# Kernel tuning notes

Measured on AMD Instinct MI355X. Metric: run time of the kernel, lower is better.

Reference implementation:

```python
import jax, jax.numpy as jnp
import numpy as np

N, D, C = 131072, 256, 1000
EPS = 1e-6


def setup_inputs() -> dict:
    key = jax.random.key(0)
    k1, k2, k3, k4 = jax.random.split(key, 4)
    feats = jax.random.normal(k1, (N, D), dtype=jnp.float32)
    pseudo_lbls = jax.random.randint(k2, (N,), 0, C)
    src_proto = jax.random.normal(k3, (C, D), dtype=jnp.float32)
    # uniform in [0.5, 1.5) to keep the Mahalanobis denominator well-conditioned
    src_proto_cov = jax.random.uniform(k4, (C, D), dtype=jnp.float32) + 0.5
    return {"feats": feats, "pseudo_lbls": pseudo_lbls,
            "src_proto": src_proto, "src_proto_cov": src_proto_cov}


def reference(feats, pseudo_lbls, src_proto, src_proto_cov):
    # Fused scatter-mean over classes (replaces the python loop over unique labels).
    num_classes, feat_dim = src_proto.shape
    counts = jax.ops.segment_sum(jnp.ones((feats.shape[0],), feats.dtype),
                                 pseudo_lbls, num_segments=num_classes)  # [C]
    sums = jax.ops.segment_sum(feats, pseudo_lbls, num_segments=num_classes)  # [C, D]
    means = sums / jnp.maximum(counts, 1.0)[:, None]                      # [C, D]
    present = counts > 0                                                  # [C]
    # GSSLoss: mean over the [n_uniq, D] elements of (mean - proto)^2 / (cov + eps)
    per_elem = (means - src_proto) ** 2 / (src_proto_cov + EPS)           # [C, D]
    per_elem = jnp.where(present[:, None], per_elem, 0.0)
    n_present = jnp.sum(present.astype(feats.dtype))
    loss = jnp.sum(per_elem) / (n_present * feat_dim)
    return loss
```

## Files before the change

### kernel.cpp

```cpp
#include <hip/hip_runtime.h>

#define EPS 1e-6f
#define MAX_C 1000
#define W 32
#define TR 128
#define RPC 4096
#define SBLK 1024


__device__ __forceinline__ void dma16(const float* g, float* l) {
    __builtin_amdgcn_global_load_lds(
        (const __attribute__((address_space(1))) unsigned int*)g,
        (__attribute__((address_space(3))) unsigned int*)l, 16, 0, 0);
}
__device__ __forceinline__ void dma4(const int* g, int* l) {
    __builtin_amdgcn_global_load_lds(
        (const __attribute__((address_space(1))) unsigned int*)g,
        (__attribute__((address_space(3))) unsigned int*)l, 4, 0, 0);
}

__global__ __launch_bounds__(SBLK)
void stream_kernel(const float* __restrict__ feats,
                   const int* __restrict__ lbls,
                   float* __restrict__ partials,
                   int* __restrict__ counts,
                   int n, int d, int nslices, int c_total) {
    int slice = blockIdx.x % nslices;
    int chunk = blockIdx.x / nslices;
    int t    = threadIdx.x;
    int wv   = t >> 6;
    int lane = t & 63;
    int half = lane >> 5;
    int col  = lane & 31;

    __shared__ float acc[MAX_C * W];
    __shared__ float stage[2][TR * W];
    __shared__ int   lbl_s[2][TR];

    int cW = c_total * W;
    int base = chunk * RPC;
    int rows = RPC; if (base + rows > n) rows = n - base;
    if (rows < 0) rows = 0;
    int ntiles = (rows + TR - 1) / TR;

    const float* fbase = feats + (size_t)base * d + slice * W;
    const int*   lbase = lbls + base;

    for (int i = t; i < cW; i += SBLK) acc[i] = 0.0f;

    if (slice == 0) {
        int* hist = (int*)&stage[0][0];
        for (int i = t; i < c_total; i += SBLK) hist[i] = 0;
        __syncthreads();
        for (int i = t; i < rows; i += SBLK) atomicAdd(&hist[lbase[i]], 1);
        __syncthreads();
        for (int i = t; i < c_total; i += SBLK) {
            int h = hist[i];
            if (h) atomicAdd(&counts[i], h);
        }
    }
    __syncthreads();

    int drow = wv * 8 + (lane >> 3);
    int dcol = (lane & 7) * 4;
    auto issue_dma = [&](int tile, int buf) {
        int r = tile * TR + drow; if (r > rows - 1) r = rows - 1;
        dma16(fbase + (size_t)r * d + dcol, &stage[buf][wv * 256]);
        if (wv == 0) {
            int r0 = tile * TR + lane;       if (r0 > rows - 1) r0 = rows - 1;
            int r1 = tile * TR + 64 + lane;  if (r1 > rows - 1) r1 = rows - 1;
            dma4(lbase + r0, &lbl_s[buf][0]);
            dma4(lbase + r1, &lbl_s[buf][64]);
        }
    };

    if (ntiles > 0) issue_dma(0, 0);

    for (int tile = 0; tile < ntiles; ++tile) {
        int cur = tile & 1;
        asm volatile("s_waitcnt vmcnt(0)" ::: "memory");
        __builtin_amdgcn_s_barrier();
        if (tile + 1 < ntiles) issue_dma(tile + 1, cur ^ 1);

        const float* stg = &stage[cur][0];
        int tb = tile * TR;
        int l0 = lbl_s[cur][lane];
        int l1 = lbl_s[cur][64 + lane];
        unsigned long long m0 = __ballot((tb + lane      < rows) && ((l0 & 15) == wv));
        unsigned long long m1 = __ballot((tb + 64 + lane < rows) && ((l1 & 15) == wv));

#define RUN(mask, lv, rbase)                                              \
        while (mask) {                                                    \
            int bA = (int)__ffsll(mask) - 1; mask &= mask - 1;            \
            int bB = -1;                                                  \
            if (mask) { bB = (int)__ffsll(mask) - 1; mask &= mask - 1; }  \
            int lA = __shfl(lv, bA);                                      \
            int lB = (bB >= 0) ? __shfl(lv, bB) : -1;                     \
            if (bB >= 0 && lB == lA) {                                    \
                if (half == 0) {                                          \
                    float v = stg[(rbase + bA) * W + col]                 \
                            + stg[(rbase + bB) * W + col];                \
                    acc[lA * W + col] += v;                               \
                }                                                         \
            } else {                                                      \
                int b_ = half ? bB : bA;                                  \
                int l_ = half ? lB : lA;                                  \
                if (b_ >= 0)                                              \
                    acc[l_ * W + col] += stg[(rbase + b_) * W + col];     \
            }                                                             \
        }
        RUN(m0, l0, 0)
        RUN(m1, l1, 64)
#undef RUN
    }
    __syncthreads();

    float* pbase = partials + (size_t)chunk * c_total * d + slice * W;
    for (int i = t; i < cW; i += SBLK) {
        int cls = i >> 5;
        int cc  = i & (W - 1);
        pbase[(size_t)cls * d + cc] = acc[i];
    }
}

__global__ __launch_bounds__(256)
void finalize_kernel(const float* __restrict__ partials,
                     const int* __restrict__ counts,
                     const float* __restrict__ proto,
                     const float* __restrict__ cov,
                     float* __restrict__ loss_acc,
                     float* __restrict__ npres_acc,
                     int* __restrict__ done,
                     float* __restrict__ out, int c_total, int d, int nchunks) {
    int c = blockIdx.x;
    int t = threadIdx.x;
    size_t idx = (size_t)c * d + t;
    size_t cstride = (size_t)c_total * d;

    float a = 0.0f;
    for (int k = 0; k < nchunks; ++k)
        a += partials[(size_t)k * cstride + idx];

    int cnt = counts[c];
    float present = (cnt > 0) ? 1.0f : 0.0f;
    float mean = a / fmaxf((float)cnt, 1.0f);
    float diff = mean - proto[idx];
    float pe = present * diff * diff / (cov[idx] + EPS);

    for (int off = 32; off > 0; off >>= 1)
        pe += __shfl_down(pe, off, 64);
    __shared__ float s[4];
    if ((t & 63) == 0) s[t >> 6] = pe;
    __syncthreads();
    if (t == 0) {
        atomicAdd(loss_acc, (s[0] + s[1]) + (s[2] + s[3]));
        atomicAdd(npres_acc, present);
        __threadfence();
        int prev = atomicAdd(done, 1);
        if (prev == c_total - 1) {
            float L = atomicAdd(loss_acc, 0.0f);
            float P = atomicAdd(npres_acc, 0.0f);
            out[0] = L / (P * (float)d);
        }
    }
}

extern "C" void kernel_launch(void* const* d_in, const int* in_sizes, int n_in,
                              void* d_out, int out_size, void* d_ws, size_t ws_size,
                              hipStream_t stream) {
    const float* feats = (const float*)d_in[0];
    const int*   lbls  = (const int*)d_in[1];
    const float* proto = (const float*)d_in[2];
    const float* cov   = (const float*)d_in[3];

    int n_rows = in_sizes[1];
    int d      = in_sizes[0] / n_rows;
    int c      = in_sizes[2] / d;

    int*   counts    = (int*)d_ws;
    float* loss_acc  = (float*)d_ws + c;
    float* npres_acc = loss_acc + 1;
    int*   done      = (int*)d_ws + c + 2;
    float* partials  = (float*)d_ws + c + 3;

    hipMemsetAsync(d_ws, 0, ((size_t)c + 3) * sizeof(int), stream);

    int nslices = d / W;
    int nchunks = (n_rows + RPC - 1) / RPC;
    stream_kernel<<<nslices * nchunks, SBLK, 0, stream>>>(
        feats, lbls, partials, counts, n_rows, d, nslices, c);
    finalize_kernel<<<c, 256, 0, stream>>>(partials, counts, proto, cov,
                                           loss_acc, npres_acc, done,
                                           (float*)d_out, c, d, nchunks);
}
```

Baseline: 270.5 us.

## Replace ballot-serialized class scatter with LDS atomics and a class-rotated layout

```diff
diff --git a/kernel.cpp b/kernel.cpp
--- a/kernel.cpp
+++ b/kernel.cpp
@@ -30,8 +30,8 @@
     int t    = threadIdx.x;
     int wv   = t >> 6;
     int lane = t & 63;
-    int half = lane >> 5;
-    int col  = lane & 31;
+    int lr   = lane >> 3;
+    int g    = lane & 7;
 
     __shared__ float acc[MAX_C * W];
     __shared__ float stage[2][TR * W];
@@ -61,11 +61,10 @@
     }
     __syncthreads();
 
-    int drow = wv * 8 + (lane >> 3);
-    int dcol = (lane & 7) * 4;
+    int drow = wv * 8 + lr;
     auto issue_dma = [&](int tile, int buf) {
         int r = tile * TR + drow; if (r > rows - 1) r = rows - 1;
-        dma16(fbase + (size_t)r * d + dcol, &stage[buf][wv * 256]);
+        dma16(fbase + (size_t)r * d + g * 4, &stage[buf][wv * 256]);
         if (wv == 0) {
             int r0 = tile * TR + lane;       if (r0 > rows - 1) r0 = rows - 1;
             int r1 = tile * TR + 64 + lane;  if (r1 > rows - 1) r1 = rows - 1;
@@ -82,44 +81,25 @@
         __builtin_amdgcn_s_barrier();
         if (tile + 1 < ntiles) issue_dma(tile + 1, cur ^ 1);
 
-        const float* stg = &stage[cur][0];
-        int tb = tile * TR;
-        int l0 = lbl_s[cur][lane];
-        int l1 = lbl_s[cur][64 + lane];
-        unsigned long long m0 = __ballot((tb + lane      < rows) && ((l0 & 15) == wv));
-        unsigned long long m1 = __ballot((tb + 64 + lane < rows) && ((l1 & 15) == wv));
-
-#define RUN(mask, lv, rbase)                                              \
-        while (mask) {                                                    \
-            int bA = (int)__ffsll(mask) - 1; mask &= mask - 1;            \
-            int bB = -1;                                                  \
-            if (mask) { bB = (int)__ffsll(mask) - 1; mask &= mask - 1; }  \
-            int lA = __shfl(lv, bA);                                      \
-            int lB = (bB >= 0) ? __shfl(lv, bB) : -1;                     \
-            if (bB >= 0 && lB == lA) {                                    \
-                if (half == 0) {                                          \
-                    float v = stg[(rbase + bA) * W + col]                 \
-                            + stg[(rbase + bB) * W + col];                \
-                    acc[lA * W + col] += v;                               \
-                }                                                         \
-            } else {                                                      \
-                int b_ = half ? bB : bA;                                  \
-                int l_ = half ? lB : lA;                                  \
-                if (b_ >= 0)                                              \
-                    acc[l_ * W + col] += stg[(rbase + b_) * W + col];     \
-            }                                                             \
+        int rglob = tile * TR + drow;
+        if (rglob < rows) {
+            float4 v = *(const float4*)&stage[cur][drow * W + g * 4];
+            int lab = lbl_s[cur][drow];
+            int b_ = lab * W, c_ = g * 4 + lab;
+            atomicAdd(&acc[b_ + ((c_ + 0) & (W - 1))], v.x);
+            atomicAdd(&acc[b_ + ((c_ + 1) & (W - 1))], v.y);
+            atomicAdd(&acc[b_ + ((c_ + 2) & (W - 1))], v.z);
+            atomicAdd(&acc[b_ + ((c_ + 3) & (W - 1))], v.w);
         }
-        RUN(m0, l0, 0)
-        RUN(m1, l1, 64)
-#undef RUN
     }
     __syncthreads();
 
     float* pbase = partials + (size_t)chunk * c_total * d + slice * W;
     for (int i = t; i < cW; i += SBLK) {
-        int cls = i >> 5;
-        int cc  = i & (W - 1);
-        pbase[(size_t)cls * d + cc] = acc[i];
+        int cls  = i >> 5;
+        int phys = i & (W - 1);
+        int lc   = (phys - cls) & (W - 1);
+        pbase[(size_t)cls * d + lc] = acc[i];
     }
 }
 
```

New measurement: 387.3 us. 43.2% more time.
